# Optimization experiments

Measured on AMD Instinct MI355X. Metric: run time of the kernel, lower is better.

Reference implementation:

```python
import jax, jax.numpy as jnp
import numpy as np

RADIUS = 0.1  # cube half-width for octant neighbor search (scalar forward arg)
_INF = jnp.float32(np.finfo(np.float32).max)


def setup_inputs() -> dict:
    key = jax.random.key(0)
    k1, k2 = jax.random.split(key)
    xyz = jax.random.uniform(k1, (2, 4096, 3), dtype=jnp.float32)   # coords in unit cube
    points = jax.random.normal(k2, (2, 4096, 64), dtype=jnp.float32)  # per-point features
    return {"xyz": xyz, "points": points}


def _select_cube(xyz, radius):
    """PointSIFT select_cube: for each point, nearest neighbor in each of the 8
    spatial octants within an axis-aligned cube of half-width `radius`.
    Falls back to the point's own index when an octant is empty.
    Returns idx [B, N, 8] int32."""
    B, N, _ = xyz.shape
    # d[b, i, j] = xyz[b, j] - xyz[b, i]
    dx = xyz[:, None, :, 0] - xyz[:, :, None, 0]  # [B, N, N]
    dy = xyz[:, None, :, 1] - xyz[:, :, None, 1]
    dz = xyz[:, None, :, 2] - xyz[:, :, None, 2]
    within = (jnp.abs(dx) < radius) & (jnp.abs(dy) < radius) & (jnp.abs(dz) < radius)
    dist = dx * dx + dy * dy + dz * dz
    octant = ((dx > 0).astype(jnp.int32) * 4
              + (dy > 0).astype(jnp.int32) * 2
              + (dz > 0).astype(jnp.int32))  # [B, N, N] in [0, 8)
    self_idx = jnp.broadcast_to(jnp.arange(N, dtype=jnp.int32)[None, :], (B, N))
    idxs = []
    for o in range(8):  # fixed small structural loop over octants
        d_o = jnp.where(within & (octant == o), dist, _INF)  # [B, N, N]
        j_o = jnp.argmin(d_o, axis=-1).astype(jnp.int32)      # [B, N]
        best = jnp.take_along_axis(d_o, j_o[..., None].astype(jnp.int32), axis=-1)[..., 0]
        idxs.append(jnp.where(best < _INF, j_o, self_idx))
    return jnp.stack(idxs, axis=-1)  # [B, N, 8]


def _group_points(t, idx):
    # t: [B, N, C], idx: [B, N, 8] -> [B, N, 8, C]
    return jax.vmap(lambda a, i: a[i])(t, idx)


def reference(xyz, points):
    idx = _select_cube(xyz, RADIUS)
    grouped_xyz = _group_points(xyz, idx) - xyz[:, :, None, :]        # center: [B,N,8,3]
    grouped_points = jnp.concatenate(
        [grouped_xyz, _group_points(points, idx)], axis=-1)           # [B,N,8,3+C]
    return grouped_xyz, grouped_points, idx
```

## Files before the change

### kernel.cpp

```cpp
#include <hip/hip_runtime.h>

#define NPTS   4096
#define CFEAT  64
#define RADIUS_F 0.1f

#define GX_SZ   (2*NPTS*8*3)
#define GP_SZ   (2*NPTS*8*67)

__global__ __launch_bounds__(512) void pointsift_fused_kernel(
    const float* __restrict__ xyz,
    const float* __restrict__ points,
    float* __restrict__ out)
{
    __shared__ float sxyz[NPTS * 3];
    __shared__ unsigned long long best[256];
    __shared__ int sj[256];

    const int t   = threadIdx.x;
    const int bid = blockIdx.x;
    const int b   = bid >> 7;
    const int base = (bid & 127) * 32;

    {
        const float4* src = (const float4*)(xyz + (size_t)b * (NPTS * 3));
        float4* dst = (float4*)sxyz;
        #pragma unroll
        for (int e = 0; e < 6; ++e) dst[t + 512 * e] = src[t + 512 * e];
    }
    if (t < 256) best[t] = ~0ull;
    __syncthreads();

    const int p  = t & 31;
    const int i  = base + p;
    const int j0 = (t >> 5) * 256;
    const float xi = sxyz[i * 3 + 0];
    const float yi = sxyz[i * 3 + 1];
    const float zi = sxyz[i * 3 + 2];

    #pragma unroll 4
    for (int jj = 0; jj < 256; ++jj) {
        const int j = j0 + jj;
        const float dx = sxyz[j * 3 + 0] - xi;
        const float dy = sxyz[j * 3 + 1] - yi;
        const float dz = sxyz[j * 3 + 2] - zi;
        if (fmaxf(fabsf(dx), fmaxf(fabsf(dy), fabsf(dz))) < RADIUS_F) {
            const float dist = __fadd_rn(__fadd_rn(__fmul_rn(dx, dx), __fmul_rn(dy, dy)),
                                         __fmul_rn(dz, dz));
            const int oct = ((dx > 0.f) ? 4 : 0) | ((dy > 0.f) ? 2 : 0) | ((dz > 0.f) ? 1 : 0);
            const unsigned long long key =
                ((unsigned long long)__float_as_uint(dist) << 32) | (unsigned int)j;
            atomicMin(&best[(oct << 5) | p], key);
        }
    }
    __syncthreads();

    float* gx_out  = out;
    float* gp_out  = out + GX_SZ;
    float* idx_out = out + GX_SZ + GP_SZ;

    if (t < 256) {
        const int o  = t & 7;
        const int pp = t >> 3;
        const int ii = base + pp;
        const unsigned long long key = best[(o << 5) | pp];
        const int j = (key == ~0ull) ? ii : (int)(unsigned int)(key & 0xFFFFFFFFull);
        sj[(o << 5) | pp] = j;
        const size_t g = ((size_t)(b * NPTS + ii) << 3) + o;
        const float gx = sxyz[j * 3 + 0] - sxyz[ii * 3 + 0];
        const float gy = sxyz[j * 3 + 1] - sxyz[ii * 3 + 1];
        const float gz = sxyz[j * 3 + 2] - sxyz[ii * 3 + 2];
        gx_out[g * 3 + 0] = gx;
        gx_out[g * 3 + 1] = gy;
        gx_out[g * 3 + 2] = gz;
        gp_out[g * 67 + 0] = gx;
        gp_out[g * 67 + 1] = gy;
        gp_out[g * 67 + 2] = gz;
        idx_out[g] = (float)j;
    }
    __syncthreads();

    const int wv   = t >> 6;
    const int lane = t & 63;
    const float* pbase = points + (size_t)b * (NPTS * CFEAT);
    for (int q = 0; q < 32; ++q) {
        const int j  = sj[(wv << 5) + q];
        const int ii = base + q;
        const size_t g = ((size_t)(b * NPTS + ii) << 3) + wv;
        gp_out[g * 67 + 3 + lane] = pbase[(size_t)j * CFEAT + lane];
    }
}

extern "C" void kernel_launch(void* const* d_in, const int* in_sizes, int n_in,
                              void* d_out, int out_size, void* d_ws, size_t ws_size,
                              hipStream_t stream) {
    const float* xyz    = (const float*)d_in[0];
    const float* points = (const float*)d_in[1];
    float* out = (float*)d_out;
    pointsift_fused_kernel<<<256, 512, 0, stream>>>(xyz, points, out);
}
```

Baseline: 85.90 us.

## Register-block four query points per thread in octant neighbor search

Each thread now holds four query points in registers and loops over candidate points with a stride of eight, instead of one query point per thread scanning 256 contiguous candidates. This reuses each candidate load from shared memory four times and so cuts LDS traffic per distance test. The lane mapping changes the LDS access pattern and atomic contention on the shared best array, since lanes that share a query can hit the same slots. It also raises register use per thread.

```diff
diff --git a/kernel.cpp b/kernel.cpp
--- a/kernel.cpp
+++ b/kernel.cpp
@@ -30,26 +30,41 @@
     if (t < 256) best[t] = ~0ull;
     __syncthreads();
 
-    const int p  = t & 31;
-    const int i  = base + p;
-    const int j0 = (t >> 5) * 256;
-    const float xi = sxyz[i * 3 + 0];
-    const float yi = sxyz[i * 3 + 1];
-    const float zi = sxyz[i * 3 + 2];
+    const int lane = t & 63;
+    const int wv   = t >> 6;
+    const int jo   = lane & 7;
+    const int qg   = lane >> 3;
+    const int q0   = qg * 4;
 
-    #pragma unroll 4
-    for (int jj = 0; jj < 256; ++jj) {
-        const int j = j0 + jj;
-        const float dx = sxyz[j * 3 + 0] - xi;
-        const float dy = sxyz[j * 3 + 1] - yi;
-        const float dz = sxyz[j * 3 + 2] - zi;
-        if (fmaxf(fabsf(dx), fmaxf(fabsf(dy), fabsf(dz))) < RADIUS_F) {
-            const float dist = __fadd_rn(__fadd_rn(__fmul_rn(dx, dx), __fmul_rn(dy, dy)),
-                                         __fmul_rn(dz, dz));
-            const int oct = ((dx > 0.f) ? 4 : 0) | ((dy > 0.f) ? 2 : 0) | ((dz > 0.f) ? 1 : 0);
-            const unsigned long long key =
-                ((unsigned long long)__float_as_uint(dist) << 32) | (unsigned int)j;
-            atomicMin(&best[(oct << 5) | p], key);
+    float qx[4], qy[4], qz[4];
+    #pragma unroll
+    for (int s = 0; s < 4; ++s) {
+        const int i = base + q0 + s;
+        qx[s] = sxyz[i * 3 + 0];
+        qy[s] = sxyz[i * 3 + 1];
+        qz[s] = sxyz[i * 3 + 2];
+    }
+
+    const int jstart = wv * 512 + jo;
+    #pragma unroll 2
+    for (int it = 0; it < 64; ++it) {
+        const int j = jstart + it * 8;
+        const float px = sxyz[j * 3 + 0];
+        const float py = sxyz[j * 3 + 1];
+        const float pz = sxyz[j * 3 + 2];
+        #pragma unroll
+        for (int s = 0; s < 4; ++s) {
+            const float dx = px - qx[s];
+            const float dy = py - qy[s];
+            const float dz = pz - qz[s];
+            if (fmaxf(fabsf(dx), fmaxf(fabsf(dy), fabsf(dz))) < RADIUS_F) {
+                const float dist = __fadd_rn(__fadd_rn(__fmul_rn(dx, dx), __fmul_rn(dy, dy)),
+                                             __fmul_rn(dz, dz));
+                const int oct = ((dx > 0.f) ? 4 : 0) | ((dy > 0.f) ? 2 : 0) | ((dz > 0.f) ? 1 : 0);
+                const unsigned long long key =
+                    ((unsigned long long)__float_as_uint(dist) << 32) | (unsigned int)j;
+                atomicMin(&best[(oct << 5) | (q0 + s)], key);
+            }
         }
     }
     __syncthreads();
@@ -79,8 +94,6 @@
     }
     __syncthreads();
 
-    const int wv   = t >> 6;
-    const int lane = t & 63;
     const float* pbase = points + (size_t)b * (NPTS * CFEAT);
     for (int q = 0; q < 32; ++q) {
         const int j  = sj[(wv << 5) + q];
```

Result: faster. 78.96 us (-8.1%).
